# Performance work log

Measured on AMD Instinct MI355X. Metric: run time of the kernel, lower is better.

## Reference

```python
import jax, jax.numpy as jnp
import numpy as np

B, S, L2 = 1, 2048, 512
DIM, HEADS, HD, FFN = 1536, 12, 128, 8960
BLK, TOPK, EPS = 64, 8, 1e-6
SCALE = HD ** -0.5

def _ln(x):
    xc = x - jnp.mean(x, -1, keepdims=True)
    return xc * jax.lax.rsqrt(jnp.mean(xc * xc, -1, keepdims=True) + EPS)

def _rms(x, w):
    return x * jax.lax.rsqrt(jnp.mean(x * x, -1, keepdims=True) + EPS) * w

def _rope(x, cos, sin):
    # is_neox_style=False: interleaved pairs
    x1, x2 = x[..., 0::2], x[..., 1::2]
    c, s = cos[None, :, None, :], sin[None, :, None, :]
    return jnp.stack([x1 * c - x2 * s, x2 * c + x1 * s], -1).reshape(x.shape)

def forward(hidden_states, encoder_hidden_states, temb, cos, sin, scale_shift_table,
            Wq, bq, Wk, bk, Wv, bv, Wg, bg, Wo, bo, qnorm_w, knorm_w, sa_ln_w, sa_ln_b,
            cWq, cbq, cWk, cbk, cWv, cbv, cWo, cbo, cqnorm_w, cknorm_w, W1, b1, W2, b2):
    e = scale_shift_table + temb  # [B,6,DIM]
    shift_msa, scale_msa, gate_msa = e[:, 0:1], e[:, 1:2], e[:, 2:3]
    c_shift, c_scale, c_gate = e[:, 3:4], e[:, 4:5], e[:, 5:6]
    norm_hs = _ln(hidden_states) * (1.0 + scale_msa) + shift_msa
    q = _rms(norm_hs @ Wq + bq, qnorm_w).reshape(B, S, HEADS, HD)
    k = _rms(norm_hs @ Wk + bk, knorm_w).reshape(B, S, HEADS, HD)
    v = (norm_hs @ Wv + bv).reshape(B, S, HEADS, HD)
    g = (norm_hs @ Wg + bg).reshape(B, S, HEADS, HD)  # gate_compress
    q, k = _rope(q, cos, sin), _rope(k, cos, sin)
    # ---- Video Sparse Attention: coarse (gated) branch + block top-k fine branch ----
    nb = S // BLK
    qc = q.reshape(B, nb, BLK, HEADS, HD).mean(2)  # cube-pooled
    kc = k.reshape(B, nb, BLK, HEADS, HD).mean(2)
    vc = v.reshape(B, nb, BLK, HEADS, HD).mean(2)
    pc = jax.nn.softmax(jnp.einsum('bnhd,bmhd->bhnm', qc, kc) * SCALE, -1)
    coarse = jnp.repeat(jnp.einsum('bhnm,bmhd->bnhd', pc, vc), BLK, axis=1)  # [B,S,H,D]
    _, idx = jax.lax.top_k(pc, TOPK)  # [B,H,nb,TOPK] selected kv blocks
    blk_mask = jax.nn.one_hot(idx, nb, dtype=jnp.float32).sum(-2) > 0  # [B,H,nb,nb]
    tok_mask = jnp.repeat(jnp.repeat(blk_mask, BLK, 2), BLK, 3)  # [B,H,S,S]
    s_fine = jnp.einsum('bshd,bthd->bhst', q, k) * SCALE
    p = jax.nn.softmax(jnp.where(tok_mask, s_fine, -1e9), -1)
    fine = jnp.einsum('bhst,bthd->bshd', p, v)
    attn = (fine + g * coarse).reshape(B, S, DIM) @ Wo + bo
    # ---- ScaleResidualLayerNormScaleShift (affine LN, null shift/scale) ----
    res = hidden_states + gate_msa * attn
    norm2 = _ln(res) * sa_ln_w + sa_ln_b
    # ---- WanT2VCrossAttention ----
    cq = _rms(norm2 @ cWq + cbq, cqnorm_w).reshape(B, S, HEADS, HD)
    ck = _rms(encoder_hidden_states @ cWk + cbk, cknorm_w).reshape(B, L2, HEADS, HD)
    cv = (encoder_hidden_states @ cWv + cbv).reshape(B, L2, HEADS, HD)
    cp = jax.nn.softmax(jnp.einsum('bshd,bthd->bhst', cq, ck) * SCALE, -1)
    cross = jnp.einsum('bhst,bthd->bshd', cp, cv).reshape(B, S, DIM) @ cWo + cbo
    res2 = res + cross
    norm3 = _ln(res2) * (1.0 + c_scale) + c_shift  # non-affine LN + scale-shift
    # ---- gelu-tanh MLP + gated residual ----
    ff = jax.nn.gelu(norm3 @ W1 + b1, approximate=True) @ W2 + b2
    return res2 + c_gate * ff

def setup_inputs():
    key = jax.random.key(0)
    ks = jax.random.split(key, 16)
    def w(i, shape, s=0.02):
        return jax.random.normal(ks[i], shape, jnp.float32) * s
    ang = jnp.arange(S, dtype=jnp.float32)[:, None] / (10000.0 ** (jnp.arange(0, HD, 2, dtype=jnp.float32) / HD))[None, :]
    z = lambda n: jnp.zeros((n,), jnp.float32)
    o = lambda n: jnp.ones((n,), jnp.float32)
    return {
        'hidden_states': jax.random.normal(ks[0], (B, S, DIM), jnp.float32),
        'encoder_hidden_states': jax.random.normal(ks[1], (B, L2, DIM), jnp.float32),
        'temb': jax.random.normal(ks[2], (B, 6, DIM), jnp.float32),
        'cos': jnp.cos(ang), 'sin': jnp.sin(ang),
        'scale_shift_table': jax.random.normal(ks[3], (1, 6, DIM), jnp.float32) / DIM ** 0.5,
        'Wq': w(4, (DIM, DIM)), 'bq': z(DIM), 'Wk': w(5, (DIM, DIM)), 'bk': z(DIM),
        'Wv': w(6, (DIM, DIM)), 'bv': z(DIM), 'Wg': w(7, (DIM, DIM)), 'bg': z(DIM),
        'Wo': w(8, (DIM, DIM)), 'bo': z(DIM),
        'qnorm_w': o(DIM), 'knorm_w': o(DIM), 'sa_ln_w': o(DIM), 'sa_ln_b': z(DIM),
        'cWq': w(9, (DIM, DIM)), 'cbq': z(DIM), 'cWk': w(10, (DIM, DIM)), 'cbk': z(DIM),
        'cWv': w(11, (DIM, DIM)), 'cbv': z(DIM), 'cWo': w(12, (DIM, DIM)), 'cbo': z(DIM),
        'cqnorm_w': o(DIM), 'cknorm_w': o(DIM),
        'W1': w(13, (DIM, FFN)), 'b1': z(FFN), 'W2': w(14, (FFN, DIM)), 'b2': z(DIM),
    }

def reference(hidden_states, encoder_hidden_states, temb, cos, sin, scale_shift_table, Wq, bq, Wk, bk, Wv, bv, Wg, bg, Wo, bo, qnorm_w, knorm_w, sa_ln_w, sa_ln_b, cWq, cbq, cWk, cbk, cWv, cbv, cWo, cbo, cqnorm_w, cknorm_w, W1, b1, W2, b2):
    return forward(hidden_states, encoder_hidden_states, temb, cos, sin, scale_shift_table, Wq, bq, Wk, bk, Wv, bv, Wg, bg, Wo, bo, qnorm_w, knorm_w, sa_ln_w, sa_ln_b, cWq, cbq, cWk, cbk, cWv, cbv, cWo, cbo, cqnorm_w, cknorm_w, W1, b1, W2, b2)
```

## Files before the change

### kernel.cpp

```cpp
#include <hip/hip_runtime.h>
#include <hip/hip_bf16.h>
#include <math.h>

#define DIMX 1536
#define SEQ 2048
#define L2X 512
#define NHEAD 12
#define HDIM 128
#define NBLK 32
#define FFNX 8960
#define SCALE_ATT 0.08838834764831845f

typedef __attribute__((ext_vector_type(4))) float f4;
typedef __attribute__((ext_vector_type(4))) float f32x4;
typedef __attribute__((ext_vector_type(8))) short bf16x8;
typedef __attribute__((ext_vector_type(4))) unsigned short us4;
typedef __attribute__((ext_vector_type(8))) unsigned short us8;
typedef unsigned short us;

static __device__ __forceinline__ us f2bf(float f) {
  union { float f; unsigned u; } v; v.f = f;
  unsigned r = v.u + 0x7FFFu + ((v.u >> 16) & 1u);
  return (us)(r >> 16);
}

static __device__ __forceinline__ void gl_lds16(const us* g, us* l) {
  __builtin_amdgcn_global_load_lds(
      (const __attribute__((address_space(1))) void*)g,
      (__attribute__((address_space(3))) void*)l, 16, 0, 0);
}

#define RAW_BAR() asm volatile("s_barrier" ::: "memory")

static __device__ __forceinline__ void xcd_map2(int& bx, int& by) {
  int gx = gridDim.x, gy = gridDim.y;
  int nwg = gx * gy;
  int lin = by * gx + bx;
  int q = nwg >> 3;
  lin = (lin & 7) * q + (lin >> 3);
  bx = lin % gx;
  by = lin / gx;
}

__global__ void __launch_bounds__(256) prep_e_kernel(const float* __restrict__ sst,
                                                     const float* __restrict__ temb,
                                                     float* __restrict__ e) {
  int i = blockIdx.x * 256 + threadIdx.x;
  if (i < 6 * DIMX) e[i] = sst[i] + temb[i];
}

struct P9 { const float* s[9]; };

__global__ void __launch_bounds__(256) pack64_9(P9 ps, us* __restrict__ dst) {
  const float* __restrict__ W = ps.s[blockIdx.z];
  us* __restrict__ Wt = dst + (size_t)blockIdx.z * DIMX * DIMX;
  __shared__ float t[64][65];
  int n0 = blockIdx.x * 64, k0 = blockIdx.y * 64;
  int tid = threadIdx.x;
#pragma unroll
  for (int i = 0; i < 4; i++) {
    int c = i * 256 + tid;
    int row = c >> 4, c4 = (c & 15) * 4;
    *reinterpret_cast<f4*>(&t[row][c4]) =
        *reinterpret_cast<const f4*>(&W[(size_t)(k0 + row) * DIMX + n0 + c4]);
  }
  __syncthreads();
#pragma unroll
  for (int i = 0; i < 2; i++) {
    int c = i * 256 + tid;
    int n = c >> 3, kc = (c & 7) * 8;
    us8 h;
#pragma unroll
    for (int j = 0; j < 8; j++) h[j] = f2bf(t[kc + j][n]);
    *reinterpret_cast<us8*>(&Wt[(size_t)(n0 + n) * DIMX + k0 + kc]) = h;
  }
}

__global__ void __launch_bounds__(256) pack64_g(const float* __restrict__ W,
                                                us* __restrict__ Wt, int K, int N) {
  __shared__ float t[64][65];
  int n0 = blockIdx.x * 64, k0 = blockIdx.y * 64;
  int tid = threadIdx.x;
#pragma unroll
  for (int i = 0; i < 4; i++) {
    int c = i * 256 + tid;
    int row = c >> 4, c4 = (c & 15) * 4;
    *reinterpret_cast<f4*>(&t[row][c4]) =
        *reinterpret_cast<const f4*>(&W[(size_t)(k0 + row) * N + n0 + c4]);
  }
  __syncthreads();
#pragma unroll
  for (int i = 0; i < 2; i++) {
    int c = i * 256 + tid;
    int n = c >> 3, kc = (c & 7) * 8;
    us8 h;
#pragma unroll
    for (int j = 0; j < 8; j++) h[j] = f2bf(t[kc + j][n]);
    *reinterpret_cast<us8*>(&Wt[(size_t)(n0 + n) * K + k0 + kc]) = h;
  }
}

__global__ void __launch_bounds__(256) pack_cvt_kernel(const float* __restrict__ X,
                                                       us* __restrict__ Y, int n4) {
  int i = blockIdx.x * 256 + threadIdx.x;
  if (i < n4) {
    f4 v = *reinterpret_cast<const f4*>(&X[(size_t)i * 4]);
    us4 h; h[0] = f2bf(v[0]); h[1] = f2bf(v[1]); h[2] = f2bf(v[2]); h[3] = f2bf(v[3]);
    *reinterpret_cast<us4*>(&Y[(size_t)i * 4]) = h;
  }
}

__global__ void __launch_bounds__(256) ln_affine_kernel(
    const float* __restrict__ X, const float* __restrict__ a,
    const float* __restrict__ b, int add1, us* __restrict__ Out) {
  __shared__ float lds4[4];
  int row = blockIdx.x, t = threadIdx.x;
  const float* x = X + (size_t)row * DIMX;
  float v[6]; float s = 0.f;
#pragma unroll
  for (int i = 0; i < 6; i++) { v[i] = x[t + 256 * i]; s += v[i]; }
  for (int o = 1; o < 64; o <<= 1) s += __shfl_xor(s, o, 64);
  if ((t & 63) == 0) lds4[t >> 6] = s;
  __syncthreads();
  float mean = (lds4[0] + lds4[1] + lds4[2] + lds4[3]) * (1.f / DIMX);
  __syncthreads();
  float s2 = 0.f;
#pragma unroll
  for (int i = 0; i < 6; i++) { float c = v[i] - mean; s2 += c * c; }
  for (int o = 1; o < 64; o <<= 1) s2 += __shfl_xor(s2, o, 64);
  if ((t & 63) == 0) lds4[t >> 6] = s2;
  __syncthreads();
  float var = (lds4[0] + lds4[1] + lds4[2] + lds4[3]) * (1.f / DIMX);
  float rstd = rsqrtf(var + 1e-6f);
#pragma unroll
  for (int i = 0; i < 6; i++) {
    int c = t + 256 * i;
    float av = a[c] + (add1 ? 1.f : 0.f);
    Out[(size_t)row * DIMX + c] = f2bf((v[i] - mean) * rstd * av + b[c]);
  }
}

__global__ void __launch_bounds__(256) reduce_ln_kernel(
    const float* __restrict__ P, const float* __restrict__ bias,
    const float* __restrict__ R, const float* __restrict__ g,
    float* __restrict__ Ores, const float* __restrict__ a,
    const float* __restrict__ b, int add1, us* __restrict__ Onorm) {
  __shared__ float lds4[4];
  int row = blockIdx.x, t = threadIdx.x;
  const size_t RN = (size_t)SEQ * DIMX;
  float v[6]; float s = 0.f;
#pragma unroll
  for (int i = 0; i < 6; i++) {
    int c = t + 256 * i;
    size_t ix = (size_t)row * DIMX + c;
    float x = P[ix];
    x += P[RN + ix]; x += P[2 * RN + ix]; x += P[3 * RN + ix];
    x += bias[c];
    x = g ? (R[ix] + g[c] * x) : (R[ix] + x);
    Ores[ix] = x;
    v[i] = x; s += x;
  }
  for (int o = 1; o < 64; o <<= 1) s += __shfl_xor(s, o, 64);
  if ((t & 63) == 0) lds4[t >> 6] = s;
  __syncthreads();
  float mean = (lds4[0] + lds4[1] + lds4[2] + lds4[3]) * (1.f / DIMX);
  __syncthreads();
  float s2 = 0.f;
#pragma unroll
  for (int i = 0; i < 6; i++) { float c = v[i] - mean; s2 += c * c; }
  for (int o = 1; o < 64; o <<= 1) s2 += __shfl_xor(s2, o, 64);
  if ((t & 63) == 0) lds4[t >> 6] = s2;
  __syncthreads();
  float var = (lds4[0] + lds4[1] + lds4[2] + lds4[3]) * (1.f / DIMX);
  float rstd = rsqrtf(var + 1e-6f);
#pragma unroll
  for (int i = 0; i < 6; i++) {
    int c = t + 256 * i;
    float av = a[c] + (add1 ? 1.f : 0.f);
    Onorm[(size_t)row * DIMX + c] = f2bf((v[i] - mean) * rstd * av + b[c]);
  }
}

__global__ void __launch_bounds__(256) rms_rope_kernel(
    float* __restrict__ X, const float* __restrict__ wgt,
    const float* __restrict__ cosT, const float* __restrict__ sinT, int do_rope,
    us* __restrict__ Ob) {
  __shared__ float lds4[4];
  int row = blockIdx.x, t = threadIdx.x;
  float* x = X + (size_t)row * DIMX;
  int base = t * 6;
  float v[6]; float s2 = 0.f;
#pragma unroll
  for (int i = 0; i < 6; i++) { v[i] = x[base + i]; s2 += v[i] * v[i]; }
  for (int o = 1; o < 64; o <<= 1) s2 += __shfl_xor(s2, o, 64);
  if ((t & 63) == 0) lds4[t >> 6] = s2;
  __syncthreads();
  float ms = (lds4[0] + lds4[1] + lds4[2] + lds4[3]) * (1.f / DIMX);
  float rstd = rsqrtf(ms + 1e-6f);
#pragma unroll
  for (int i = 0; i < 6; i++) v[i] *= rstd * wgt[base + i];
  if (do_rope) {
#pragma unroll
    for (int j = 0; j < 3; j++) {
      int c = base + 2 * j;
      int pi = (c & (HDIM - 1)) >> 1;
      float cs = cosT[row * (HDIM / 2) + pi], sn = sinT[row * (HDIM / 2) + pi];
      float ev = v[2 * j], ov = v[2 * j + 1];
      v[2 * j] = ev * cs - ov * sn;
      v[2 * j + 1] = ov * cs + ev * sn;
    }
  }
#pragma unroll
  for (int i = 0; i < 6; i++) {
    x[base + i] = v[i];
    Ob[(size_t)row * DIMX + base + i] = f2bf(v[i]);
  }
}

struct Outs {
  float *o0, *o1, *o2, *o3;
  const float *b0, *b1, *b2, *b3;
  us* ob;
};

template<int NP, int NCHUNK, int OUT_BF16, int DO_GELU, int SPLITK>
__global__ void __launch_bounds__(512, 2) gemm2ph(
    const us* __restrict__ A, const us* __restrict__ Bt,
    Outs outs, int M, int N, int K, int Kfull) {
  constexpr int NT = NP * 32;
  constexpr int TOT = 16384 + NT * 64;
  constexpr int BI = (NT * 8 + 511) / 512;
  constexpr int NH0 = NP / 2;
  constexpr int NH1 = NP - NH0;
  __shared__ __align__(16) us S[2 * TOT];
  const int tid = threadIdx.x;
  const int lane = tid & 63;
  const int wid = tid >> 6;
  const int wr = wid >> 1, wc = wid & 1;
  const int fr = lane & 15, xo = lane >> 4;
  const int r7 = fr & 7, q4 = xo * 4;
  int bx = blockIdx.x, by = blockIdx.y;
  xcd_map2(bx, by);
  const int tm = by * 256, tn = bx * NT;
  const size_t kb = SPLITK ? (size_t)blockIdx.z * K : 0;

  auto stA = [&](int buf, int k0) {
#pragma unroll
    for (int i = 0; i < 4; i++) {
      int c = i * 512 + tid;
      gl_lds16(A + (size_t)(tm + (c >> 3)) * Kfull + kb + k0 + (((c & 7) ^ ((c >> 3) & 7)) * 8),
               S + buf * TOT + (i * 512 + wid * 64) * 8);
    }
  };
  auto stB = [&](int buf, int k0) {
#pragma unroll
    for (int i = 0; i < BI; i++) {
      int c = i * 512 + tid;
      if (c < NT * 8)
        gl_lds16(Bt + (size_t)(tn + (c >> 3)) * Kfull + kb + k0 + (((c & 7) ^ ((c >> 3) & 7)) * 8),
                 S + buf * TOT + 16384 + (i * 512 + wid * 64) * 8);
    }
  };
  auto rdA = [&](int buf, int mp, int ks) -> bf16x8 {
    int r = wr * 64 + mp * 16 + fr;
    int ko = ((ks * 4 + xo) ^ r7) * 8;
    return *reinterpret_cast<const bf16x8*>(&S[buf * TOT + r * 64 + ko]);
  };
  auto rdB = [&](int buf, int np, int ks) -> bf16x8 {
    int r = wc * (NP * 16) + np * 16 + fr;
    int ko = ((ks * 4 + xo) ^ r7) * 8;
    return *reinterpret_cast<const bf16x8*>(&S[buf * TOT + 16384 + r * 64 + ko]);
  };

  f32x4 acc[4][NP];
#pragma unroll
  for (int m = 0; m < 4; m++)
#pragma unroll
    for (int n = 0; n < NP; n++) acc[m][n] = (f32x4)(0.f);
  bf16x8 aF[2][4], bFr[2][NH1 > NH0 ? NH1 : NH0];

  const int nt = K >> 6;
  stA(0, 0); stB(0, 0); stA(1, 64);
  asm volatile("s_waitcnt vmcnt(4)" ::: "memory");
  RAW_BAR();

  for (int t = 0; t < nt; t++) {
    const int buf = t & 1;
    const int k1 = (t + 1) << 6, k2 = (t + 2) << 6;
#pragma unroll
    for (int ks = 0; ks < 2; ks++)
#pragma unroll
      for (int m = 0; m < 4; m++) aF[ks][m] = rdA(buf, m, ks);
#pragma unroll
    for (int ks = 0; ks < 2; ks++)
#pragma unroll
      for (int n = 0; n < NH0; n++) bFr[ks][n] = rdB(buf, n, ks);
    if (t + 1 < nt) stB(buf ^ 1, k1);
    RAW_BAR();
    __builtin_amdgcn_s_setprio(1);
#pragma unroll
    for (int ks = 0; ks < 2; ks++)
#pragma unroll
      for (int m = 0; m < 4; m++)
#pragma unroll
        for (int n = 0; n < NH0; n++)
          acc[m][n] = __builtin_amdgcn_mfma_f32_16x16x32_bf16(aF[ks][m], bFr[ks][n], acc[m][n], 0, 0, 0);
    __builtin_amdgcn_s_setprio(0);
    RAW_BAR();
#pragma unroll
    for (int ks = 0; ks < 2; ks++)
#pragma unroll
      for (int n = 0; n < NH1; n++) bFr[ks][n] = rdB(buf, NH0 + n, ks);
    if (t + 2 < nt) stA(buf, k2);
    RAW_BAR();
    __builtin_amdgcn_s_setprio(1);
#pragma unroll
    for (int ks = 0; ks < 2; ks++)
#pragma unroll
      for (int m = 0; m < 4; m++)
#pragma unroll
        for (int n = 0; n < NH1; n++)
          acc[m][NH0 + n] = __builtin_amdgcn_mfma_f32_16x16x32_bf16(aF[ks][m], bFr[ks][n], acc[m][NH0 + n], 0, 0, 0);
    __builtin_amdgcn_s_setprio(0);
    if (t + 2 < nt) asm volatile("s_waitcnt vmcnt(4)" ::: "memory");
    else            asm volatile("s_waitcnt vmcnt(0)" ::: "memory");
    RAW_BAR();
  }

#pragma unroll
  for (int m = 0; m < 4; m++)
#pragma unroll
    for (int n = 0; n < NP; n++) {
      int col = tn + wc * (NP * 16) + n * 16 + fr;
      int rowb = tm + wr * 64 + m * 16 + q4;
      if (SPLITK) {
        float* P = outs.o0 + (size_t)blockIdx.z * M * N;
#pragma unroll
        for (int r = 0; r < 4; r++)
          P[(size_t)(rowb + r) * N + col] = acc[m][n][r];
      } else {
        int c2; float* op; const float* bp; int sel = 0;
        if constexpr (NCHUNK == 1) {
          c2 = col; op = outs.o0; bp = outs.b0;
        } else {
          sel = col >= 3 * DIMX ? 3 : (col >= 2 * DIMX ? 2 : (col >= DIMX ? 1 : 0));
          c2 = col - sel * DIMX;
          op = sel == 0 ? outs.o0 : (sel == 1 ? outs.o1 : (sel == 2 ? outs.o2 : outs.o3));
          bp = sel == 0 ? outs.b0 : (sel == 1 ? outs.b1 : (sel == 2 ? outs.b2 : outs.b3));
        }
        float bv = bp[c2];
#pragma unroll
        for (int r = 0; r < 4; r++) {
          float v = acc[m][n][r] + bv;
          if (DO_GELU) {
            float u = 1.5957691216057308f * (v + 0.044715f * v * v * v);
            v = v / (1.f + __expf(-u));
          }
          if (OUT_BF16)
            outs.ob[(size_t)(rowb + r) * N + col] = f2bf(v);
          else {
            op[(size_t)(rowb + r) * DIMX + c2] = v;
            if (NCHUNK == 4 && outs.ob != nullptr && sel == 2)
              outs.ob[(size_t)(rowb + r) * DIMX + c2] = f2bf(v);
          }
        }
      }
    }
}

__global__ void __launch_bounds__(512, 2) gemm10(
    const us* __restrict__ A, const us* __restrict__ Bt,
    const float* __restrict__ bias, us* __restrict__ Cb,
    int M, int N, int K) {
  constexpr int NT = 320;
  constexpr int TOT = 16384 + NT * 64;
  __shared__ __align__(16) us S[2 * TOT];
  const int tid = threadIdx.x;
  const int lane = tid & 63;
  const int wid = tid >> 6;
  const int wr = wid >> 2, wc = wid & 3;
  const int fr = lane & 15, xo = lane >> 4;
  const int r7 = fr & 7, q4 = xo * 4;
  int bx = blockIdx.x, by = blockIdx.y;
  xcd_map2(bx, by);
  const int tm = by * 256, tn = bx * NT;

  auto stA = [&](int buf, int k0) {
#pragma unroll
    for (int i = 0; i < 4; i++) {
      int c = i * 512 + tid;
      gl_lds16(A + (size_t)(tm + (c >> 3)) * K + k0 + (((c & 7) ^ ((c >> 3) & 7)) * 8),
               S + buf * TOT + (i * 512 + wid * 64) * 8);
    }
  };
  auto stB = [&](int buf, int k0) {
#pragma unroll
    for (int i = 0; i < 5; i++) {
      int c = i * 512 + tid;
      gl_lds16(Bt + (size_t)(tn + (c >> 3)) * K + k0 + (((c & 7) ^ ((c >> 3) & 7)) * 8),
               S + buf * TOT + 16384 + (i * 512 + wid * 64) * 8);
    }
  };
  auto rdA = [&](int buf, int mp, int ks) -> bf16x8 {
    int r = wr * 128 + mp * 16 + fr;
    int ko = ((ks * 4 + xo) ^ r7) * 8;
    return *reinterpret_cast<const bf16x8*>(&S[buf * TOT + r * 64 + ko]);
  };
  auto rdB = [&](int buf, int np, int ks) -> bf16x8 {
    int r = wc * 80 + np * 16 + fr;
    int ko = ((ks * 4 + xo) ^ r7) * 8;
    return *reinterpret_cast<const bf16x8*>(&S[buf * TOT + 16384 + r * 64 + ko]);
  };

  f32x4 acc[8][5];
#pragma unroll
  for (int m = 0; m < 8; m++)
#pragma unroll
    for (int n = 0; n < 5; n++) acc[m][n] = (f32x4)(0.f);
  bf16x8 aF[8], bF[5];

  const int nt = K >> 6;
  stA(0, 0); stB(0, 0); stA(1, 64);
  asm volatile("s_waitcnt vmcnt(4)" ::: "memory");
  RAW_BAR();

  for (int t = 0; t < nt; t++) {
    const int buf = t & 1;
    const int k1 = (t + 1) << 6, k2 = (t + 2) << 6;
#pragma unroll
    for (int m = 0; m < 8; m++) aF[m] = rdA(buf, m, 0);
#pragma unroll
    for (int n = 0; n < 5; n++) bF[n] = rdB(buf, n, 0);
    if (t + 1 < nt) stB(buf ^ 1, k1);
    RAW_BAR();
    __builtin_amdgcn_s_setprio(1);
#pragma unroll
    for (int m = 0; m < 8; m++)
#pragma unroll
      for (int n = 0; n < 5; n++)
        acc[m][n] = __builtin_amdgcn_mfma_f32_16x16x32_bf16(aF[m], bF[n], acc[m][n], 0, 0, 0);
    __builtin_amdgcn_s_setprio(0);
    RAW_BAR();
#pragma unroll
    for (int m = 0; m < 8; m++) aF[m] = rdA(buf, m, 1);
#pragma unroll
    for (int n = 0; n < 5; n++) bF[n] = rdB(buf, n, 1);
    if (t + 2 < nt) stA(buf, k2);
    RAW_BAR();
    __builtin_amdgcn_s_setprio(1);
#pragma unroll
    for (int m = 0; m < 8; m++)
#pragma unroll
      for (int n = 0; n < 5; n++)
        acc[m][n] = __builtin_amdgcn_mfma_f32_16x16x32_bf16(aF[m], bF[n], acc[m][n], 0, 0, 0);
    __builtin_amdgcn_s_setprio(0);
    if (t + 2 < nt) asm volatile("s_waitcnt vmcnt(4)" ::: "memory");
    else            asm volatile("s_waitcnt vmcnt(0)" ::: "memory");
    RAW_BAR();
  }

#pragma unroll
  for (int m = 0; m < 8; m++)
#pragma unroll
    for (int n = 0; n < 5; n++) {
      int col = tn + wc * 80 + n * 16 + fr;
      int rowb = tm + wr * 128 + m * 16 + q4;
      float bv = bias[col];
#pragma unroll
      for (int r = 0; r < 4; r++) {
        float v = acc[m][n][r] + bv;
        float u = 1.5957691216057308f * (v + 0.044715f * v * v * v);
        v = v / (1.f + __expf(-u));
        Cb[(size_t)(rowb + r) * N + col] = f2bf(v);
      }
    }
}

template<int NCHUNK>
__global__ void __launch_bounds__(256) gemm_multi(
    const us* __restrict__ A, const us* __restrict__ Bt,
    Outs outs, int M, int N, int K) {
  __shared__ __align__(16) us As[128 * 64];
  __shared__ __align__(16) us Bs[128 * 64];
  const int tid = threadIdx.x;
  const int lane = tid & 63;
  const int w = tid >> 6;
  const int wr = w >> 1, wc = w & 1;
  const int fr = lane & 15;
  const int xo = lane >> 4;
  const int r7 = fr & 7;
  const int q4 = xo * 4;
  int bx = blockIdx.x, by = blockIdx.y;
  xcd_map2(bx, by);
  const int tm = by * 128, tn = bx * 128;

  f32x4 acc[4][4];
#pragma unroll
  for (int m = 0; m < 4; m++)
#pragma unroll
    for (int n = 0; n < 4; n++) acc[m][n] = (f32x4)(0.f);

  int srow[4], skc[4];
#pragma unroll
  for (int j = 0; j < 4; j++) {
    int c = j * 256 + tid;
    srow[j] = c >> 3;
    skc[j] = ((c & 7) ^ ((c >> 3) & 7)) * 8;
  }

  for (int k0 = 0; k0 < K; k0 += 64) {
#pragma unroll
    for (int j = 0; j < 4; j++) {
      gl_lds16(A + (size_t)(tm + srow[j]) * K + k0 + skc[j], As + (j * 256 + w * 64) * 8);
      gl_lds16(Bt + (size_t)(tn + srow[j]) * K + k0 + skc[j], Bs + (j * 256 + w * 64) * 8);
    }
    __syncthreads();
    bf16x8 af[2][4], bfv[2][4];
#pragma unroll
    for (int ks = 0; ks < 2; ks++) {
      const int koff = (((ks * 4 + xo) ^ r7) << 3);
#pragma unroll
      for (int m = 0; m < 4; m++)
        af[ks][m] = *reinterpret_cast<const bf16x8*>(&As[(wr * 64 + m * 16 + fr) * 64 + koff]);
#pragma unroll
      for (int n = 0; n < 4; n++)
        bfv[ks][n] = *reinterpret_cast<const bf16x8*>(&Bs[(wc * 64 + n * 16 + fr) * 64 + koff]);
    }
#pragma unroll
    for (int ks = 0; ks < 2; ks++)
#pragma unroll
      for (int m = 0; m < 4; m++)
#pragma unroll
        for (int n = 0; n < 4; n++)
          acc[m][n] = __builtin_amdgcn_mfma_f32_16x16x32_bf16(af[ks][m], bfv[ks][n], acc[m][n], 0, 0, 0);
    __syncthreads();
  }
#pragma unroll
  for (int m = 0; m < 4; m++) {
#pragma unroll
    for (int n = 0; n < 4; n++) {
      int col = tn + wc * 64 + n * 16 + fr;
      int c2; float* op; const float* bp;
      if constexpr (NCHUNK == 2) {
        int sel = col >= DIMX;
        c2 = col - sel * DIMX;
        op = sel ? outs.o1 : outs.o0;
        bp = sel ? outs.b1 : outs.b0;
      } else {
        c2 = col; op = outs.o0; bp = outs.b0;
      }
      float bv = bp[c2];
#pragma unroll
      for (int r = 0; r < 4; r++) {
        int row = tm + wr * 64 + m * 16 + q4 + r;
        op[(size_t)row * DIMX + c2] = acc[m][n][r] + bv;
      }
    }
  }
}

template<int S>
__global__ void __launch_bounds__(256) reduce_kernel(
    const float* __restrict__ P, const float* __restrict__ bias,
    const float* __restrict__ R, const float* __restrict__ g,
    float* __restrict__ O, int total4, int ncol4) {
  const f4* P4 = (const f4*)P;
  const f4* R4 = (const f4*)R;
  f4* O4 = (f4*)O;
  for (int i = blockIdx.x * 256 + threadIdx.x; i < total4; i += gridDim.x * 256) {
    f4 s = P4[i];
#pragma unroll
    for (int sl = 1; sl < S; sl++) s += P4[(size_t)sl * total4 + i];
    int c4 = (i % ncol4) * 4;
    s += *reinterpret_cast<const f4*>(&bias[c4]);
    if (R) {
      if (g) {
        f4 gv = *reinterpret_cast<const f4*>(&g[c4]);
        s = R4[i] + gv * s;
      } else {
        s = R4[i] + s;
      }
    }
    O4[i] = s;
  }
}

__global__ void __launch_bounds__(256) attn_kernel(
    const us* __restrict__ Q, const us* __restrict__ Kx,
    const us* __restrict__ V, const int* __restrict__ idx,
    const float* __restrict__ G, const float* __restrict__ CB,
    us* __restrict__ Out) {
  __shared__ us q_s[64 * 136];
  __shared__ us k_s[64 * 136];
  __shared__ us vT_s[128 * 72];
  __shared__ us p_s[64 * 72];
  __shared__ float red[4 * 64];
  __shared__ float m_run[64], l_run[64], alpha_s[64];

  const int qb = blockIdx.x;
  const int h = blockIdx.y;
  const int tid = threadIdx.x;
  const int lane = tid & 63;
  const int w = tid >> 6;
  const int fr = lane & 15;
  const int k8 = (lane >> 4) * 8;
  const int q4 = (lane >> 4) * 4;

#pragma unroll
  for (int i = 0; i < 4; i++) {
    int c = i * 256 + tid;
    int row = c >> 4, d8 = (c & 15) * 8;
    us8 v = *reinterpret_cast<const us8*>(&Q[(size_t)(qb * 64 + row) * DIMX + h * HDIM + d8]);
    *reinterpret_cast<us8*>(&q_s[row * 136 + d8]) = v;
  }
  if (tid < 64) { m_run[tid] = -1e30f; l_run[tid] = 0.f; }

  f32x4 acc_o[4][2];
#pragma unroll
  for (int m = 0; m < 4; m++)
#pragma unroll
    for (int n = 0; n < 2; n++) acc_o[m][n] = (f32x4)(0.f);

  for (int ib = 0; ib < 8; ib++) {
    int blk = idx ? idx[(h * NBLK + qb) * 8 + ib] : ib;
    __syncthreads();
#pragma unroll
    for (int i = 0; i < 4; i++) {
      int c = i * 256 + tid;
      int row = c >> 4, d8 = (c & 15) * 8;
      us8 v = *reinterpret_cast<const us8*>(&Kx[(size_t)(blk * 64 + row) * DIMX + h * HDIM + d8]);
      *reinterpret_cast<us8*>(&k_s[row * 136 + d8]) = v;
    }
    {
      int d = tid & 127, th = (tid >> 7) * 32;
#pragma unroll
      for (int j = 0; j < 4; j++) {
        us8 hv;
#pragma unroll
        for (int qq = 0; qq < 8; qq++)
          hv[qq] = V[(size_t)(blk * 64 + th + j * 8 + qq) * DIMX + h * HDIM + d];
        *reinterpret_cast<us8*>(&vT_s[d * 72 + th + j * 8]) = hv;
      }
    }
    __syncthreads();
    f32x4 accs[4];
#pragma unroll
    for (int m = 0; m < 4; m++) accs[m] = (f32x4)(0.f);
#pragma unroll
    for (int kk = 0; kk < 128; kk += 32) {
      bf16x8 bfr = *reinterpret_cast<const bf16x8*>(&k_s[(w * 16 + fr) * 136 + kk + k8]);
#pragma unroll
      for (int m = 0; m < 4; m++) {
        bf16x8 afr = *reinterpret_cast<const bf16x8*>(&q_s[(m * 16 + fr) * 136 + kk + k8]);
        accs[m] = __builtin_amdgcn_mfma_f32_16x16x32_bf16(afr, bfr, accs[m], 0, 0, 0);
      }
    }
#pragma unroll
    for (int m = 0; m < 4; m++) {
#pragma unroll
      for (int r = 0; r < 4; r++) {
        accs[m][r] *= SCALE_ATT;
        float v = accs[m][r];
        for (int o = 1; o < 16; o <<= 1) v = fmaxf(v, __shfl_xor(v, o, 64));
        if (fr == 0) red[w * 64 + m * 16 + q4 + r] = v;
      }
    }
    __syncthreads();
    if (tid < 64) {
      float bm = fmaxf(fmaxf(red[tid], red[64 + tid]), fmaxf(red[128 + tid], red[192 + tid]));
      float mo = m_run[tid];
      float mn = fmaxf(mo, bm);
      float al = __expf(mo - mn);
      alpha_s[tid] = al;
      m_run[tid] = mn;
      l_run[tid] *= al;
    }
    __syncthreads();
#pragma unroll
    for (int m = 0; m < 4; m++) {
#pragma unroll
      for (int r = 0; r < 4; r++) {
        int row = m * 16 + q4 + r;
        float p = __expf(accs[m][r] - m_run[row]);
        p_s[row * 72 + w * 16 + fr] = f2bf(p);
        float sv = p;
        for (int o = 1; o < 16; o <<= 1) sv += __shfl_xor(sv, o, 64);
        if (fr == 0) red[w * 64 + row] = sv;
      }
    }
#pragma unroll
    for (int m = 0; m < 4; m++) {
      float a0 = alpha_s[m * 16 + q4 + 0];
      float a1 = alpha_s[m * 16 + q4 + 1];
      float a2 = alpha_s[m * 16 + q4 + 2];
      float a3 = alpha_s[m * 16 + q4 + 3];
#pragma unroll
      for (int n = 0; n < 2; n++) {
        acc_o[m][n][0] *= a0; acc_o[m][n][1] *= a1;
        acc_o[m][n][2] *= a2; acc_o[m][n][3] *= a3;
      }
    }
    __syncthreads();
    if (tid < 64) l_run[tid] += red[tid] + red[64 + tid] + red[128 + tid] + red[192 + tid];
#pragma unroll
    for (int kk = 0; kk < 64; kk += 32) {
      bf16x8 pa[4];
#pragma unroll
      for (int m = 0; m < 4; m++)
        pa[m] = *reinterpret_cast<const bf16x8*>(&p_s[(m * 16 + fr) * 72 + kk + k8]);
#pragma unroll
      for (int n = 0; n < 2; n++) {
        bf16x8 vb = *reinterpret_cast<const bf16x8*>(&vT_s[(w * 32 + n * 16 + fr) * 72 + kk + k8]);
#pragma unroll
        for (int m = 0; m < 4; m++)
          acc_o[m][n] = __builtin_amdgcn_mfma_f32_16x16x32_bf16(pa[m], vb, acc_o[m][n], 0, 0, 0);
      }
    }
  }
  __syncthreads();
#pragma unroll
  for (int m = 0; m < 4; m++) {
#pragma unroll
    for (int n = 0; n < 2; n++) {
#pragma unroll
      for (int r = 0; r < 4; r++) {
        int row = m * 16 + q4 + r;
        int srow = qb * 64 + row;
        int d = w * 32 + n * 16 + fr;
        float o = acc_o[m][n][r] / l_run[row];
        size_t oi = (size_t)srow * DIMX + h * HDIM + d;
        if (G) o += G[oi] * CB[(size_t)qb * DIMX + h * HDIM + d];
        Out[oi] = f2bf(o);
      }
    }
  }
}

__global__ void __launch_bounds__(128) block_mean3_kernel(const float* __restrict__ q,
                                                          const float* __restrict__ k,
                                                          const float* __restrict__ v,
                                                          float* __restrict__ qc,
                                                          float* __restrict__ kc,
                                                          float* __restrict__ vc) {
  int n = blockIdx.x, h = blockIdx.y, z = blockIdx.z, d = threadIdx.x;
  const float* X = z == 0 ? q : (z == 1 ? k : v);
  float* O = z == 0 ? qc : (z == 1 ? kc : vc);
  float s = 0.f;
  for (int t = 0; t < 64; t++) s += X[(size_t)(n * 64 + t) * DIMX + h * HDIM + d];
  O[(n * NHEAD + h) * HDIM + d] = s * (1.f / 64.f);
}

__global__ void __launch_bounds__(256) coarse_attn_kernel(const float* __restrict__ qc,
                                                          const float* __restrict__ kc,
                                                          float* __restrict__ pc,
                                                          int* __restrict__ idxout) {
  int h = blockIdx.x, t = threadIdx.x;
  __shared__ float sm[32][32];
  for (int p = t; p < 1024; p += 256) {
    int n = p >> 5, m = p & 31;
    float dot = 0.f;
    for (int d = 0; d < HDIM; d++)
      dot += qc[n * DIMX + h * HDIM + d] * kc[m * DIMX + h * HDIM + d];
    sm[n][m] = dot * SCALE_ATT;
  }
  __syncthreads();
  if (t < 32) {
    int n = t;
    float mx = -1e30f;
#pragma unroll
    for (int m = 0; m < 32; m++) mx = fmaxf(mx, sm[n][m]);
    float pv[32]; float ssum = 0.f;
#pragma unroll
    for (int m = 0; m < 32; m++) { pv[m] = __expf(sm[n][m] - mx); ssum += pv[m]; }
    float inv = 1.f / ssum;
#pragma unroll
    for (int m = 0; m < 32; m++) { pv[m] *= inv; pc[(h * 32 + n) * 32 + m] = pv[m]; }
    unsigned chosen = 0;
    for (int i = 0; i < 8; i++) {
      float best = -1.f; int bi = 0;
#pragma unroll
      for (int m = 0; m < 32; m++)
        if (!((chosen >> m) & 1u) && pv[m] > best) { best = pv[m]; bi = m; }
      chosen |= 1u << bi;
      idxout[(h * 32 + n) * 8 + i] = bi;
    }
  }
}

__global__ void __launch_bounds__(128) coarse_ctx_kernel(const float* __restrict__ pc,
                                                         const float* __restrict__ vc,
                                                         float* __restrict__ cb) {
  int n = blockIdx.x, h = blockIdx.y, d = threadIdx.x;
  float s = 0.f;
  for (int m = 0; m < 32; m++)
    s += pc[(h * 32 + n) * 32 + m] * vc[(m * NHEAD + h) * HDIM + d];
  cb[(n * NHEAD + h) * HDIM + d] = s;
}

extern "C" void kernel_launch(void* const* d_in, const int* in_sizes, int n_in,
                              void* d_out, int out_size, void* d_ws, size_t ws_size,
                              hipStream_t stream) {
  (void)in_sizes; (void)n_in; (void)out_size; (void)ws_size;
  const float* hidden = (const float*)d_in[0];
  const float* enc    = (const float*)d_in[1];
  const float* temb   = (const float*)d_in[2];
  const float* cosT   = (const float*)d_in[3];
  const float* sinT   = (const float*)d_in[4];
  const float* sst    = (const float*)d_in[5];
  const float* Wq = (const float*)d_in[6];   const float* bq = (const float*)d_in[7];
  const float* Wk = (const float*)d_in[8];   const float* bk = (const float*)d_in[9];
  const float* Wv = (const float*)d_in[10];  const float* bv = (const float*)d_in[11];
  const float* Wg = (const float*)d_in[12];  const float* bg = (const float*)d_in[13];
  const float* Wo = (const float*)d_in[14];  const float* bo = (const float*)d_in[15];
  const float* qnw = (const float*)d_in[16]; const float* knw = (const float*)d_in[17];
  const float* saw = (const float*)d_in[18]; const float* sab = (const float*)d_in[19];
  const float* cWq = (const float*)d_in[20]; const float* cbq = (const float*)d_in[21];
  const float* cWk = (const float*)d_in[22]; const float* cbk = (const float*)d_in[23];
  const float* cWv = (const float*)d_in[24]; const float* cbv = (const float*)d_in[25];
  const float* cWo = (const float*)d_in[26]; const float* cbo = (const float*)d_in[27];
  const float* cqnw = (const float*)d_in[28]; const float* cknw = (const float*)d_in[29];
  const float* W1 = (const float*)d_in[30];  const float* b1 = (const float*)d_in[31];
  const float* W2 = (const float*)d_in[32];  const float* b2 = (const float*)d_in[33];

  char* ws = (char*)d_ws;
  size_t off = 0;
  auto alloc = [&](size_t bytes) -> void* {
    void* p = ws + off;
    off += (bytes + 255) & ~(size_t)255;
    return p;
  };
  const size_t SD = (size_t)SEQ * DIMX * 4;
  const size_t SDh = (size_t)SEQ * DIMX * 2;
  const size_t WSQ = (size_t)DIMX * DIMX * 2;
  float* e     = (float*)alloc(6 * DIMX * 4);
  us* normb    = (us*)alloc(SDh);
  float* qb_   = (float*)alloc(SD);
  float* kb_   = (float*)alloc(SD);
  float* vb_   = (float*)alloc(SD);
  float* gb_   = (float*)alloc(SD);
  us* qbh      = (us*)alloc(SDh);
  us* kbh      = (us*)alloc(SDh);
  us* vbh      = (us*)alloc(SDh);
  float* qc    = (float*)alloc((size_t)NBLK * DIMX * 4);
  float* kc    = (float*)alloc((size_t)NBLK * DIMX * 4);
  float* vc    = (float*)alloc((size_t)NBLK * DIMX * 4);
  float* pc    = (float*)alloc(NHEAD * 32 * 32 * 4);
  int*   idx   = (int*)alloc(NHEAD * 32 * 8 * 4);
  float* cb    = (float*)alloc((size_t)NBLK * DIMX * 4);
  us* mixb     = (us*)alloc(SDh);
  float* res   = (float*)alloc(SD);
  us* encb     = (us*)alloc((size_t)L2X * DIMX * 2);
  us* wpack    = (us*)alloc(9 * WSQ);
  us* W1t      = (us*)alloc((size_t)DIMX * FFNX * 2);
  us* W2t      = (us*)alloc((size_t)FFNX * DIMX * 2);
  us* ffh    = (us*)qb_;
  us* crossb = mixb;
  float* part4q = qb_;
  float* part4w = (float*)wpack;
  float* outf  = (float*)d_out;
  const size_t SL = (size_t)DIMX * DIMX;
  us* Wot  = wpack + 4 * SL;
  us* cWqt = wpack + 5 * SL;
  us* cKVt = wpack + 6 * SL;
  us* cWot = wpack + 8 * SL;

  P9 p9; p9.s[0]=Wq; p9.s[1]=Wk; p9.s[2]=Wv; p9.s[3]=Wg; p9.s[4]=Wo;
  p9.s[5]=cWq; p9.s[6]=cWk; p9.s[7]=cWv; p9.s[8]=cWo;
  pack64_9<<<dim3(DIMX / 64, DIMX / 64, 9), 256, 0, stream>>>(p9, wpack);
  pack64_g<<<dim3(FFNX / 64, DIMX / 64), 256, 0, stream>>>(W1, W1t, DIMX, FFNX);
  pack64_g<<<dim3(DIMX / 64, FFNX / 64), 256, 0, stream>>>(W2, W2t, FFNX, DIMX);
  pack_cvt_kernel<<<(L2X * DIMX / 4 + 255) / 256, 256, 0, stream>>>(enc, encb, L2X * DIMX / 4);
  prep_e_kernel<<<36, 256, 0, stream>>>(sst, temb, e);

  ln_affine_kernel<<<SEQ, 256, 0, stream>>>(hidden, e + DIMX, e, 1, normb);
  Outs qkvgo = {qb_, kb_, vb_, gb_, bq, bk, bv, bg, vbh};
  gemm2ph<6, 4, 0, 0, 0><<<dim3(32, 8), 512, 0, stream>>>(normb, wpack, qkvgo, SEQ, 4 * DIMX, DIMX, DIMX);
  rms_rope_kernel<<<SEQ, 256, 0, stream>>>(qb_, qnw, cosT, sinT, 1, qbh);
  rms_rope_kernel<<<SEQ, 256, 0, stream>>>(kb_, knw, cosT, sinT, 1, kbh);
  block_mean3_kernel<<<dim3(NBLK, NHEAD, 3), 128, 0, stream>>>(qb_, kb_, vb_, qc, kc, vc);
  coarse_attn_kernel<<<NHEAD, 256, 0, stream>>>(qc, kc, pc, idx);
  coarse_ctx_kernel<<<dim3(NBLK, NHEAD), 128, 0, stream>>>(pc, vc, cb);
  attn_kernel<<<dim3(NBLK, NHEAD), 256, 0, stream>>>(qbh, kbh, vbh, idx, gb_, cb, mixb);
  Outs wo_o = {part4q, nullptr, nullptr, nullptr, nullptr, nullptr, nullptr, nullptr, nullptr};
  gemm2ph<6, 1, 0, 0, 1><<<dim3(8, 8, 4), 512, 0, stream>>>(mixb, Wot, wo_o, SEQ, DIMX, 384, DIMX);
  reduce_ln_kernel<<<SEQ, 256, 0, stream>>>(part4q, bo, hidden, e + 2 * DIMX,
                                            res, saw, sab, 0, normb);
  gemm2ph<6, 1, 0, 0, 1><<<dim3(8, 8, 4), 512, 0, stream>>>(normb, cWqt, wo_o, SEQ, DIMX, 384, DIMX);
  reduce_kernel<4><<<1024, 256, 0, stream>>>(part4q, cbq, nullptr, nullptr, qb_,
                                             SEQ * DIMX / 4, DIMX / 4);
  rms_rope_kernel<<<SEQ, 256, 0, stream>>>(qb_, cqnw, cosT, sinT, 0, qbh);
  Outs ckvo = {kb_, vb_, nullptr, nullptr, cbk, cbv, nullptr, nullptr, nullptr};
  gemm_multi<2><<<dim3(24, 4), 256, 0, stream>>>(encb, cKVt, ckvo, L2X, 2 * DIMX, DIMX);
  rms_rope_kernel<<<L2X, 256, 0, stream>>>(kb_, cknw, cosT, sinT, 0, kbh);
  pack_cvt_kernel<<<(L2X * DIMX / 4 + 255) / 256, 256, 0, stream>>>(vb_, vbh, L2X * DIMX / 4);
  attn_kernel<<<dim3(NBLK, NHEAD), 256, 0, stream>>>(qbh, kbh, vbh, nullptr, nullptr, nullptr, crossb);
  gemm2ph<6, 1, 0, 0, 1><<<dim3(8, 8, 4), 512, 0, stream>>>(crossb, cWot, wo_o, SEQ, DIMX, 384, DIMX);
  reduce_ln_kernel<<<SEQ, 256, 0, stream>>>(part4q, cbo, res, nullptr,
                                            outf, e + 4 * DIMX, e + 3 * DIMX, 1, normb);
  gemm10<<<dim3(28, 8), 512, 0, stream>>>(normb, W1t, b1, ffh, SEQ, FFNX, DIMX);
  Outs f2o = {part4w, nullptr, nullptr, nullptr, nullptr, nullptr, nullptr, nullptr, nullptr};
  gemm2ph<6, 1, 0, 0, 1><<<dim3(8, 8, 4), 512, 0, stream>>>(ffh, W2t, f2o, SEQ, DIMX, 2240, FFNX);
  reduce_kernel<4><<<1024, 256, 0, stream>>>(part4w, b2, outf, e + 5 * DIMX, outf,
                                             SEQ * DIMX / 4, DIMX / 4);
}
```

Baseline: 588.0 us.

## Partition attention work by query rows per wave to drop block-wide softmax syncs

Reworks the sparse attention kernel so each wave owns 16 query rows across all keys and head dims, instead of 16 keys or 32 dims across all 64 query rows. Q fragments stay in registers and softmax max and sum statistics are reduced entirely with intra-wave shuffles. This removes the shared reduction buffers and three block-wide barriers per KV block, and gives each wave a private P tile. In exchange each wave holds 8 output accumulators and re-reads every K row from LDS, which raises register use.

```diff
diff --git a/kernel.cpp b/kernel.cpp
--- a/kernel.cpp
+++ b/kernel.cpp
@@ -590,12 +590,9 @@
     const us* __restrict__ V, const int* __restrict__ idx,
     const float* __restrict__ G, const float* __restrict__ CB,
     us* __restrict__ Out) {
-  __shared__ us q_s[64 * 136];
   __shared__ us k_s[64 * 136];
   __shared__ us vT_s[128 * 72];
-  __shared__ us p_s[64 * 72];
-  __shared__ float red[4 * 64];
-  __shared__ float m_run[64], l_run[64], alpha_s[64];
+  __shared__ us p_s[4][16 * 72];
 
   const int qb = blockIdx.x;
   const int h = blockIdx.y;
@@ -603,23 +600,22 @@
   const int lane = tid & 63;
   const int w = tid >> 6;
   const int fr = lane & 15;
-  const int k8 = (lane >> 4) * 8;
-  const int q4 = (lane >> 4) * 4;
-
-#pragma unroll
-  for (int i = 0; i < 4; i++) {
-    int c = i * 256 + tid;
-    int row = c >> 4, d8 = (c & 15) * 8;
-    us8 v = *reinterpret_cast<const us8*>(&Q[(size_t)(qb * 64 + row) * DIMX + h * HDIM + d8]);
-    *reinterpret_cast<us8*>(&q_s[row * 136 + d8]) = v;
-  }
-  if (tid < 64) { m_run[tid] = -1e30f; l_run[tid] = 0.f; }
-
-  f32x4 acc_o[4][2];
-#pragma unroll
-  for (int m = 0; m < 4; m++)
-#pragma unroll
-    for (int n = 0; n < 2; n++) acc_o[m][n] = (f32x4)(0.f);
+  const int xo = lane >> 4;
+  const int k8 = xo * 8;
+  const int q4 = xo * 4;
+
+  bf16x8 qF[4];
+#pragma unroll
+  for (int kk = 0; kk < 4; kk++)
+    qF[kk] = *reinterpret_cast<const bf16x8*>(
+        &Q[(size_t)(qb * 64 + w * 16 + fr) * DIMX + h * HDIM + kk * 32 + k8]);
+
+  float m_[4], l_[4];
+#pragma unroll
+  for (int r = 0; r < 4; r++) { m_[r] = -1e30f; l_[r] = 0.f; }
+  f32x4 acc[8];
+#pragma unroll
+  for (int n = 0; n < 8; n++) acc[n] = (f32x4)(0.f);
 
   for (int ib = 0; ib < 8; ib++) {
     int blk = idx ? idx[(h * NBLK + qb) * 8 + ib] : ib;
@@ -645,95 +641,71 @@
     __syncthreads();
     f32x4 accs[4];
 #pragma unroll
-    for (int m = 0; m < 4; m++) accs[m] = (f32x4)(0.f);
-#pragma unroll
-    for (int kk = 0; kk < 128; kk += 32) {
-      bf16x8 bfr = *reinterpret_cast<const bf16x8*>(&k_s[(w * 16 + fr) * 136 + kk + k8]);
-#pragma unroll
-      for (int m = 0; m < 4; m++) {
-        bf16x8 afr = *reinterpret_cast<const bf16x8*>(&q_s[(m * 16 + fr) * 136 + kk + k8]);
-        accs[m] = __builtin_amdgcn_mfma_f32_16x16x32_bf16(afr, bfr, accs[m], 0, 0, 0);
+    for (int n = 0; n < 4; n++) accs[n] = (f32x4)(0.f);
+#pragma unroll
+    for (int kk = 0; kk < 4; kk++)
+#pragma unroll
+      for (int n = 0; n < 4; n++) {
+        bf16x8 kb = *reinterpret_cast<const bf16x8*>(&k_s[(n * 16 + fr) * 136 + kk * 32 + k8]);
+        accs[n] = __builtin_amdgcn_mfma_f32_16x16x32_bf16(qF[kk], kb, accs[n], 0, 0, 0);
       }
-    }
-#pragma unroll
-    for (int m = 0; m < 4; m++) {
+#pragma unroll
+    for (int n = 0; n < 4; n++)
+#pragma unroll
+      for (int r = 0; r < 4; r++) accs[n][r] *= SCALE_ATT;
+    float al[4];
+#pragma unroll
+    for (int r = 0; r < 4; r++) {
+      float v = fmaxf(fmaxf(accs[0][r], accs[1][r]), fmaxf(accs[2][r], accs[3][r]));
+      for (int o = 1; o < 16; o <<= 1) v = fmaxf(v, __shfl_xor(v, o, 64));
+      float mn = fmaxf(m_[r], v);
+      al[r] = __expf(m_[r] - mn);
+      m_[r] = mn;
+      l_[r] *= al[r];
+    }
+    float ps[4] = {0.f, 0.f, 0.f, 0.f};
+#pragma unroll
+    for (int n = 0; n < 4; n++)
 #pragma unroll
       for (int r = 0; r < 4; r++) {
-        accs[m][r] *= SCALE_ATT;
-        float v = accs[m][r];
-        for (int o = 1; o < 16; o <<= 1) v = fmaxf(v, __shfl_xor(v, o, 64));
-        if (fr == 0) red[w * 64 + m * 16 + q4 + r] = v;
+        float p = __expf(accs[n][r] - m_[r]);
+        p_s[w][(q4 + r) * 72 + n * 16 + fr] = f2bf(p);
+        ps[r] += p;
       }
-    }
-    __syncthreads();
-    if (tid < 64) {
-      float bm = fmaxf(fmaxf(red[tid], red[64 + tid]), fmaxf(red[128 + tid], red[192 + tid]));
-      float mo = m_run[tid];
-      float mn = fmaxf(mo, bm);
-      float al = __expf(mo - mn);
-      alpha_s[tid] = al;
-      m_run[tid] = mn;
-      l_run[tid] *= al;
-    }
-    __syncthreads();
-#pragma unroll
-    for (int m = 0; m < 4; m++) {
-#pragma unroll
-      for (int r = 0; r < 4; r++) {
-        int row = m * 16 + q4 + r;
-        float p = __expf(accs[m][r] - m_run[row]);
-        p_s[row * 72 + w * 16 + fr] = f2bf(p);
-        float sv = p;
-        for (int o = 1; o < 16; o <<= 1) sv += __shfl_xor(sv, o, 64);
-        if (fr == 0) red[w * 64 + row] = sv;
+#pragma unroll
+    for (int r = 0; r < 4; r++) {
+      float sv = ps[r];
+      for (int o = 1; o < 16; o <<= 1) sv += __shfl_xor(sv, o, 64);
+      l_[r] += sv;
+    }
+#pragma unroll
+    for (int n = 0; n < 8; n++) {
+      acc[n][0] *= al[0]; acc[n][1] *= al[1];
+      acc[n][2] *= al[2]; acc[n][3] *= al[3];
+    }
+    bf16x8 pa[2];
+#pragma unroll
+    for (int ks = 0; ks < 2; ks++)
+      pa[ks] = *reinterpret_cast<const bf16x8*>(&p_s[w][fr * 72 + ks * 32 + k8]);
+#pragma unroll
+    for (int ks = 0; ks < 2; ks++)
+#pragma unroll
+      for (int n = 0; n < 8; n++) {
+        bf16x8 vb = *reinterpret_cast<const bf16x8*>(&vT_s[(n * 16 + fr) * 72 + ks * 32 + k8]);
+        acc[n] = __builtin_amdgcn_mfma_f32_16x16x32_bf16(pa[ks], vb, acc[n], 0, 0, 0);
       }
-    }
-#pragma unroll
-    for (int m = 0; m < 4; m++) {
-      float a0 = alpha_s[m * 16 + q4 + 0];
-      float a1 = alpha_s[m * 16 + q4 + 1];
-      float a2 = alpha_s[m * 16 + q4 + 2];
-      float a3 = alpha_s[m * 16 + q4 + 3];
-#pragma unroll
-      for (int n = 0; n < 2; n++) {
-        acc_o[m][n][0] *= a0; acc_o[m][n][1] *= a1;
-        acc_o[m][n][2] *= a2; acc_o[m][n][3] *= a3;
-      }
-    }
-    __syncthreads();
-    if (tid < 64) l_run[tid] += red[tid] + red[64 + tid] + red[128 + tid] + red[192 + tid];
-#pragma unroll
-    for (int kk = 0; kk < 64; kk += 32) {
-      bf16x8 pa[4];
-#pragma unroll
-      for (int m = 0; m < 4; m++)
-        pa[m] = *reinterpret_cast<const bf16x8*>(&p_s[(m * 16 + fr) * 72 + kk + k8]);
-#pragma unroll
-      for (int n = 0; n < 2; n++) {
-        bf16x8 vb = *reinterpret_cast<const bf16x8*>(&vT_s[(w * 32 + n * 16 + fr) * 72 + kk + k8]);
-#pragma unroll
-        for (int m = 0; m < 4; m++)
-          acc_o[m][n] = __builtin_amdgcn_mfma_f32_16x16x32_bf16(pa[m], vb, acc_o[m][n], 0, 0, 0);
-      }
-    }
-  }
-  __syncthreads();
-#pragma unroll
-  for (int m = 0; m < 4; m++) {
-#pragma unroll
-    for (int n = 0; n < 2; n++) {
-#pragma unroll
-      for (int r = 0; r < 4; r++) {
-        int row = m * 16 + q4 + r;
-        int srow = qb * 64 + row;
-        int d = w * 32 + n * 16 + fr;
-        float o = acc_o[m][n][r] / l_run[row];
-        size_t oi = (size_t)srow * DIMX + h * HDIM + d;
-        if (G) o += G[oi] * CB[(size_t)qb * DIMX + h * HDIM + d];
-        Out[oi] = f2bf(o);
-      }
-    }
-  }
+  }
+#pragma unroll
+  for (int n = 0; n < 8; n++)
+#pragma unroll
+    for (int r = 0; r < 4; r++) {
+      int srow = qb * 64 + w * 16 + q4 + r;
+      int d = n * 16 + fr;
+      float o = acc[n][r] / l_[r];
+      size_t oi = (size_t)srow * DIMX + h * HDIM + d;
+      if (G) o += G[oi] * CB[(size_t)qb * DIMX + h * HDIM + d];
+      Out[oi] = f2bf(o);
+    }
 }
 
 __global__ void __launch_bounds__(128) block_mean3_kernel(const float* __restrict__ q,
```

After: 552.2 us. 6.1% less time.
